# Kernel optimization log

Hardware: AMD Instinct MI355X
Metric: run time of the kernel (lower is better)

Reference implementation:

```python
import jax, jax.numpy as jnp
import numpy as np

B, H, W = 8, 64, 64
DIM_RGB, DIM_PL, EMBED, OUT = 256, 256, 128, 256
BN_EPS = 1e-5


def conv1x1(x, w, b=None):
    # x: (B,C,H,W), w: (D,C) -> (B,D,H,W)
    y = jnp.einsum('bchw,dc->bdhw', x, w)
    if b is not None:
        y = y + b[None, :, None, None]
    return y


def spatial_attention(q, k, v, scale):
    # q,k,v: (B,D,H,W)
    b, d, h, w = q.shape
    n = h * w
    qf = q.reshape(b, d, n).transpose(0, 2, 1)   # (B,N,D)
    kf = k.reshape(b, d, n)                       # (B,D,N)
    vf = v.reshape(b, d, n).transpose(0, 2, 1)   # (B,N,D)
    attn = jax.nn.softmax(jnp.einsum('bnd,bdm->bnm', qf, kf) * scale, axis=-1)
    out = jnp.einsum('bnm,bmd->bnd', attn, vf)   # (B,N,D)
    return out.transpose(0, 2, 1).reshape(b, d, h, w)


def setup_inputs() -> dict:
    key = jax.random.key(0)
    ks = jax.random.split(key, 20)
    s = 0.05
    inp = {
        'f_rgb': jax.random.normal(ks[0], (B, DIM_RGB, H, W), jnp.float32),
        'f_pl': jax.random.normal(ks[1], (B, DIM_PL, H, W), jnp.float32),
        'w_q_rgb': jax.random.normal(ks[2], (EMBED, DIM_RGB), jnp.float32) * s,
        'b_q_rgb': jax.random.normal(ks[3], (EMBED,), jnp.float32) * s,
        'w_k_pl': jax.random.normal(ks[4], (EMBED, DIM_PL), jnp.float32) * s,
        'b_k_pl': jax.random.normal(ks[5], (EMBED,), jnp.float32) * s,
        'w_v_pl': jax.random.normal(ks[6], (EMBED, DIM_PL), jnp.float32) * s,
        'b_v_pl': jax.random.normal(ks[7], (EMBED,), jnp.float32) * s,
        'w_q_pl': jax.random.normal(ks[8], (EMBED, DIM_PL), jnp.float32) * s,
        'b_q_pl': jax.random.normal(ks[9], (EMBED,), jnp.float32) * s,
        'w_k_rgb': jax.random.normal(ks[10], (EMBED, DIM_RGB), jnp.float32) * s,
        'b_k_rgb': jax.random.normal(ks[11], (EMBED,), jnp.float32) * s,
        'w_v_rgb': jax.random.normal(ks[12], (EMBED, DIM_RGB), jnp.float32) * s,
        'b_v_rgb': jax.random.normal(ks[13], (EMBED,), jnp.float32) * s,
        'w_proj': jax.random.normal(ks[14], (OUT, 2 * EMBED), jnp.float32) * s,
        'bn_gamma': jnp.ones((OUT,), jnp.float32),
        'bn_beta': jnp.zeros((OUT,), jnp.float32),
        'bn_mean': jax.random.normal(ks[15], (OUT,), jnp.float32) * 0.01,
        'bn_var': jax.random.uniform(ks[16], (OUT,), jnp.float32, 0.5, 1.5),
    }
    return inp


def reference(f_rgb, f_pl, w_q_rgb, b_q_rgb, w_k_pl, b_k_pl, w_v_pl, b_v_pl,
              w_q_pl, b_q_pl, w_k_rgb, b_k_rgb, w_v_rgb, b_v_rgb,
              w_proj, bn_gamma, bn_beta, bn_mean, bn_var):
    scale = EMBED ** -0.5
    out_rgb2pl = spatial_attention(
        conv1x1(f_rgb, w_q_rgb, b_q_rgb),
        conv1x1(f_pl, w_k_pl, b_k_pl),
        conv1x1(f_pl, w_v_pl, b_v_pl), scale)
    out_pl2rgb = spatial_attention(
        conv1x1(f_pl, w_q_pl, b_q_pl),
        conv1x1(f_rgb, w_k_rgb, b_k_rgb),
        conv1x1(f_rgb, w_v_rgb, b_v_rgb), scale)
    combined = jnp.concatenate([out_rgb2pl, out_pl2rgb], axis=1)  # (B,2E,H,W)
    y = conv1x1(combined, w_proj)  # no bias
    # BatchNorm2d (inference form) + ReLU
    inv = bn_gamma * jax.lax.rsqrt(bn_var + BN_EPS)
    y = y * inv[None, :, None, None] + (bn_beta - bn_mean * inv)[None, :, None, None]
    return jax.nn.relu(y)
```

## Files before the change

### kernel.cpp

```cpp
#include <hip/hip_runtime.h>
#include <hip/hip_bf16.h>
#include <hip/hip_fp16.h>

typedef _Float16 f16;
typedef _Float16 f16x8 __attribute__((ext_vector_type(8)));
typedef _Float16 f16x4 __attribute__((ext_vector_type(4)));
typedef float f32x4 __attribute__((ext_vector_type(4)));
typedef float f32x16 __attribute__((ext_vector_type(16)));

#define NP   4096
#define NB   8
#define CINC 256
#define EMB  128
#define OUTC 256
#define BN_EPS 1e-5f

#define DSZ  ((size_t)NB * NP * EMB)
#define TSZ  (2 * DSZ)

__global__ __launch_bounds__(256) void proj_all_kernel(
    const float* __restrict__ Xrgb, const float* __restrict__ Xpl,
    const float* __restrict__ w0, const float* __restrict__ b0,
    const float* __restrict__ w1, const float* __restrict__ b1,
    const float* __restrict__ w2, const float* __restrict__ b2,
    const float* __restrict__ w3, const float* __restrict__ b3,
    const float* __restrict__ w4, const float* __restrict__ b4,
    const float* __restrict__ w5, const float* __restrict__ b5,
    f16* __restrict__ Qt, f16* __restrict__ Kt, f16* __restrict__ Vn)
{
    const int m0 = blockIdx.x * 128;
    const int p  = blockIdx.y;
    const int b  = blockIdx.z;
    const int s  = (p >= 3) ? 1 : 0;
    const int j  = p - s * 3;
    const int tid = threadIdx.x;
    const int w = tid >> 6, lane = tid & 63, quad = lane >> 4, lr = lane & 15;

    const float* X  = s ? Xpl : Xrgb;
    const float* W  = p == 0 ? w0 : p == 1 ? w1 : p == 2 ? w2
                    : p == 3 ? w3 : p == 4 ? w4 : w5;
    const float* Bi = p == 0 ? b0 : p == 1 ? b1 : p == 2 ? b2
                    : p == 3 ? b3 : p == 4 ? b4 : b5;

    __shared__ __align__(16) f16 smem[128 * 72 * 2];
    f16* Al = smem;
    f16* Bl = smem + 128 * 72;

    f32x4 acc[2][8];
    #pragma unroll
    for (int mi = 0; mi < 2; ++mi)
        #pragma unroll
        for (int ni = 0; ni < 8; ++ni) acc[mi][ni] = (f32x4){0.f, 0.f, 0.f, 0.f};

    for (int kt = 0; kt < 4; ++kt) {
        const int kc0 = kt * 64;
        __syncthreads();
        for (int s2 = tid; s2 < 1024; s2 += 256) {
            const int n = s2 & 127, cg = s2 >> 7;
            f16 tmp[8];
            #pragma unroll
            for (int jj = 0; jj < 8; ++jj)
                tmp[jj] = (f16)X[((size_t)b * CINC + kc0 + cg * 8 + jj) * NP + m0 + n];
            *(f16x8*)&Al[n * 72 + cg * 8] = *(const f16x8*)tmp;
        }
        for (int s2 = tid; s2 < 1024; s2 += 256) {
            const int d = s2 >> 3, cg = s2 & 7;
            f16 tmp[8];
            #pragma unroll
            for (int jj = 0; jj < 8; ++jj)
                tmp[jj] = (f16)W[(size_t)d * CINC + kc0 + cg * 8 + jj];
            *(f16x8*)&Bl[d * 72 + cg * 8] = *(const f16x8*)tmp;
        }
        __syncthreads();
        #pragma unroll
        for (int ks = 0; ks < 2; ++ks) {
            f16x8 af[2], bfr[8];
            #pragma unroll
            for (int mi = 0; mi < 2; ++mi)
                af[mi] = *(const f16x8*)&Al[(w * 32 + mi * 16 + lr) * 72 + ks * 32 + quad * 8];
            #pragma unroll
            for (int ni = 0; ni < 8; ++ni)
                bfr[ni] = *(const f16x8*)&Bl[(ni * 16 + lr) * 72 + ks * 32 + quad * 8];
            #pragma unroll
            for (int mi = 0; mi < 2; ++mi)
                #pragma unroll
                for (int ni = 0; ni < 8; ++ni)
                    acc[mi][ni] = __builtin_amdgcn_mfma_f32_16x16x32_f16(
                        af[mi], bfr[ni], acc[mi][ni], 0, 0, 0);
        }
    }

    float bias[8];
    #pragma unroll
    for (int ni = 0; ni < 8; ++ni) bias[ni] = Bi[ni * 16 + lr];

    if (j < 2) {
        f16* out = (j == 0) ? (Qt + (size_t)s * DSZ) : (Kt + (size_t)(1 - s) * DSZ);
        #pragma unroll
        for (int mi = 0; mi < 2; ++mi)
            #pragma unroll
            for (int ni = 0; ni < 8; ++ni)
                #pragma unroll
                for (int r = 0; r < 4; ++r) {
                    const int n = m0 + w * 32 + mi * 16 + quad * 4 + r;
                    out[((size_t)b * NP + n) * EMB + ni * 16 + lr] =
                        (f16)(acc[mi][ni][r] + bias[ni]);
                }
    } else {
        f16* outV = Vn + (size_t)(1 - s) * DSZ;
        __syncthreads();
        f16* T = smem;
        #pragma unroll
        for (int mi = 0; mi < 2; ++mi)
            #pragma unroll
            for (int ni = 0; ni < 8; ++ni)
                #pragma unroll
                for (int r = 0; r < 4; ++r)
                    T[(ni * 16 + lr) * 136 + w * 32 + mi * 16 + quad * 4 + r] =
                        (f16)(acc[mi][ni][r] + bias[ni]);
        __syncthreads();
        for (int s2 = tid; s2 < 2048; s2 += 256) {
            const int d = s2 >> 4, n8 = (s2 & 15) * 8;
            *(f16x8*)&outV[((size_t)b * EMB + d) * NP + m0 + n8] =
                *(const f16x8*)&T[d * 136 + n8];
        }
    }
}

__device__ __forceinline__ unsigned pkf16(float a, float b) {
    union { f16 h[2]; unsigned u; } t;
    t.h[0] = (f16)a; t.h[1] = (f16)b;
    return t.u;
}

__global__ __launch_bounds__(256, 1) void attn_kernel(
    const f16* __restrict__ Qt, const f16* __restrict__ Kt,
    const f16* __restrict__ Vn, f16* __restrict__ combT)
{
    const int bid = blockIdx.x;
    const int g = bid & 15, dir = g >> 3, b = g & 7;
    const int n0 = (bid >> 4) * 256;
    const int tid = threadIdx.x;
    const int w = tid >> 6, lane = tid & 63;
    const int l31 = lane & 31, hi = lane >> 5;

    const f16* __restrict__ Q = Qt + ((size_t)dir * NB + b) * NP * EMB;
    const f16* __restrict__ K = Kt + ((size_t)dir * NB + b) * NP * EMB;
    const f16* __restrict__ V = Vn + ((size_t)dir * NB + b) * (size_t)EMB * NP;

    __shared__ __align__(16) f16 Kl[2][64 * 128];
    __shared__ __align__(16) f16 Vl[2][128 * 64];

    const int qbase = n0 + w * 64;

    f16x8 qf[2][8];
    #pragma unroll
    for (int q32 = 0; q32 < 2; ++q32)
        #pragma unroll
        for (int d16 = 0; d16 < 8; ++d16) {
            f16x8 q = *(const f16x8*)&Q[(size_t)(qbase + q32 * 32 + l31) * EMB + d16 * 16 + hi * 8];
            #pragma unroll
            for (int jj = 0; jj < 8; ++jj)
                q[jj] = q[jj] * (f16)0.12752749f;
            qf[q32][d16] = q;
        }

    f32x16 O[4][2];
    #pragma unroll
    for (int d32 = 0; d32 < 4; ++d32)
        #pragma unroll
        for (int q32 = 0; q32 < 2; ++q32) O[d32][q32] = (f32x16)(0.0f);
    float rs[2] = {0.f, 0.f};

    const int krp = lane >> 4, kp = lane & 15;
    const int vrp = lane >> 3, vp = lane & 7;
    f16x8 stK[4], stV[4];

    auto stage_load = [&](int m0) {
        #pragma unroll
        for (int i = 0; i < 4; ++i) {
            const int r = w * 16 + i * 4 + krp;
            const int c = kp ^ (r & 7);
            stK[i] = *(const f16x8*)&K[(size_t)(m0 + r) * EMB + c * 8];
        }
        #pragma unroll
        for (int i = 0; i < 4; ++i) {
            const int r = w * 32 + i * 8 + vrp;
            const int c = vp ^ (r & 7);
            stV[i] = *(const f16x8*)&V[(size_t)r * NP + m0 + c * 8];
        }
    };
    auto stage_write = [&](int buf) {
        #pragma unroll
        for (int i = 0; i < 4; ++i) {
            const int r = w * 16 + i * 4 + krp;
            *(f16x8*)&Kl[buf][r * 128 + kp * 8] = stK[i];
        }
        #pragma unroll
        for (int i = 0; i < 4; ++i) {
            const int r = w * 32 + i * 8 + vrp;
            *(f16x8*)&Vl[buf][r * 64 + vp * 8] = stV[i];
        }
    };

    stage_load(0);
    stage_write(0);
    int cur = 0;

    for (int t = 0; t < NP / 64; ++t) {
        __syncthreads();
        if (t < NP / 64 - 1) stage_load((t + 1) * 64);

        const f16* Kb = &Kl[cur][0];
        const f16* Vb = &Vl[cur][0];

        #pragma unroll
        for (int k32 = 0; k32 < 2; ++k32) {
            f32x16 s0 = (f32x16)(0.0f), s1 = (f32x16)(0.0f);
            #pragma unroll
            for (int d16 = 0; d16 < 8; ++d16) {
                const int r = k32 * 32 + l31;
                const int c = (d16 * 2 + hi) ^ (r & 7);
                const f16x8 kf = *(const f16x8*)&Kb[r * 128 + c * 8];
                s0 = __builtin_amdgcn_mfma_f32_32x32x16_f16(kf, qf[0][d16], s0, 0, 0, 0);
                s1 = __builtin_amdgcn_mfma_f32_32x32x16_f16(kf, qf[1][d16], s1, 0, 0, 0);
            }

            f16x8 pb[2][2];
            #pragma unroll
            for (int q32 = 0; q32 < 2; ++q32) {
                const f32x16 s = q32 ? s1 : s0;
                float e[16];
                #pragma unroll
                for (int i = 0; i < 16; ++i) e[i] = __builtin_amdgcn_exp2f(s[i]);
                float sum = 0.f;
                #pragma unroll
                for (int i = 0; i < 16; ++i) sum += e[i];
                rs[q32] += sum;
                #pragma unroll
                for (int g2 = 0; g2 < 2; ++g2) {
                    const unsigned pa  = pkf16(e[g2 * 8 + 0], e[g2 * 8 + 1]);
                    const unsigned pbu = pkf16(e[g2 * 8 + 2], e[g2 * 8 + 3]);
                    const unsigned pc  = pkf16(e[g2 * 8 + 4], e[g2 * 8 + 5]);
                    const unsigned pd  = pkf16(e[g2 * 8 + 6], e[g2 * 8 + 7]);
                    const unsigned recv0 = __shfl_xor(hi ? pa : pc, 32);
                    const unsigned recv1 = __shfl_xor(hi ? pbu : pd, 32);
                    union { unsigned u[4]; f16x8 v; } pu;
                    pu.u[0] = hi ? recv0 : pa;
                    pu.u[1] = hi ? recv1 : pbu;
                    pu.u[2] = hi ? pc : recv0;
                    pu.u[3] = hi ? pd : recv1;
                    pb[g2][q32] = pu.v;
                }
            }

            #pragma unroll
            for (int g2 = 0; g2 < 2; ++g2) {
                #pragma unroll
                for (int d32 = 0; d32 < 4; ++d32) {
                    const int r = d32 * 32 + l31;
                    const int c = ((k32 * 2 + g2) * 2 + hi) ^ (r & 7);
                    const f16x8 vf = *(const f16x8*)&Vb[r * 64 + c * 8];
                    O[d32][0] = __builtin_amdgcn_mfma_f32_32x32x16_f16(vf, pb[g2][0], O[d32][0], 0, 0, 0);
                    O[d32][1] = __builtin_amdgcn_mfma_f32_32x32x16_f16(vf, pb[g2][1], O[d32][1], 0, 0, 0);
                }
            }
        }

        if (t < NP / 64 - 1) stage_write(cur ^ 1);
        cur ^= 1;
    }

    rs[0] += __shfl_xor(rs[0], 32);
    rs[1] += __shfl_xor(rs[1], 32);
    const float inv[2] = {1.0f / rs[0], 1.0f / rs[1]};
    #pragma unroll
    for (int q32 = 0; q32 < 2; ++q32) {
        const int n = qbase + q32 * 32 + l31;
        #pragma unroll
        for (int d32 = 0; d32 < 4; ++d32)
            #pragma unroll
            for (int tq = 0; tq < 4; ++tq) {
                f16 o4[4];
                #pragma unroll
                for (int jj = 0; jj < 4; ++jj)
                    o4[jj] = (f16)(O[d32][q32][tq * 4 + jj] * inv[q32]);
                *(f16x4*)&combT[((size_t)b * NP + n) * OUTC + dir * EMB + d32 * 32 + tq * 8 + hi * 4] =
                    *(const f16x4*)o4;
            }
    }
}

__global__ __launch_bounds__(256) void proj_out_kernel(
    const f16* __restrict__ combT, const float* __restrict__ Wp,
    const float* __restrict__ G, const float* __restrict__ Be,
    const float* __restrict__ Mu, const float* __restrict__ Va,
    float* __restrict__ out)
{
    const int m0 = blockIdx.x * 128;
    const int o0 = blockIdx.y * 128;
    const int b  = blockIdx.z;
    const int tid = threadIdx.x;
    const int w = tid >> 6, lane = tid & 63, quad = lane >> 4, lr = lane & 15;

    __shared__ __align__(16) f16 smem[128 * 72 * 2];
    f16* Al = smem;
    f16* Bl = smem + 128 * 72;

    f32x4 acc[2][8];
    #pragma unroll
    for (int mi = 0; mi < 2; ++mi)
        #pragma unroll
        for (int ni = 0; ni < 8; ++ni) acc[mi][ni] = (f32x4){0.f, 0.f, 0.f, 0.f};

    for (int kt = 0; kt < 4; ++kt) {
        const int kc0 = kt * 64;
        __syncthreads();
        #pragma unroll
        for (int i = 0; i < 4; ++i) {
            const int s2 = i * 256 + tid;
            const int n = s2 >> 3, cg = s2 & 7;
            *(f16x8*)&Al[n * 72 + cg * 8] =
                *(const f16x8*)&combT[((size_t)b * NP + m0 + n) * OUTC + kc0 + cg * 8];
        }
        for (int s2 = tid; s2 < 1024; s2 += 256) {
            const int d = s2 >> 3, cg = s2 & 7;
            f16 tmp[8];
            #pragma unroll
            for (int jj = 0; jj < 8; ++jj)
                tmp[jj] = (f16)Wp[(size_t)(o0 + d) * OUTC + kc0 + cg * 8 + jj];
            *(f16x8*)&Bl[d * 72 + cg * 8] = *(const f16x8*)tmp;
        }
        __syncthreads();
        #pragma unroll
        for (int ks = 0; ks < 2; ++ks) {
            f16x8 af[2], bfr[8];
            #pragma unroll
            for (int mi = 0; mi < 2; ++mi)
                af[mi] = *(const f16x8*)&Al[(w * 32 + mi * 16 + lr) * 72 + ks * 32 + quad * 8];
            #pragma unroll
            for (int ni = 0; ni < 8; ++ni)
                bfr[ni] = *(const f16x8*)&Bl[(ni * 16 + lr) * 72 + ks * 32 + quad * 8];
            #pragma unroll
            for (int mi = 0; mi < 2; ++mi)
                #pragma unroll
                for (int ni = 0; ni < 8; ++ni)
                    acc[mi][ni] = __builtin_amdgcn_mfma_f32_16x16x32_f16(
                        af[mi], bfr[ni], acc[mi][ni], 0, 0, 0);
        }
    }

    __syncthreads();
    f16* T = smem;
    #pragma unroll
    for (int ni = 0; ni < 8; ++ni) {
        const int o = o0 + ni * 16 + lr;
        const float iv = G[o] * rsqrtf(Va[o] + BN_EPS);
        const float sh = Be[o] - Mu[o] * iv;
        #pragma unroll
        for (int mi = 0; mi < 2; ++mi)
            #pragma unroll
            for (int r = 0; r < 4; ++r)
                T[(ni * 16 + lr) * 136 + w * 32 + mi * 16 + quad * 4 + r] =
                    (f16)fmaxf(acc[mi][ni][r] * iv + sh, 0.f);
    }
    __syncthreads();
    for (int s2 = tid; s2 < 2048; s2 += 256) {
        const int o = s2 >> 4, n8 = (s2 & 15) * 8;
        const f16x8 v = *(const f16x8*)&T[o * 136 + n8];
        const size_t off = ((size_t)b * OUTC + o0 + o) * NP + m0 + n8;
        #pragma unroll
        for (int k = 0; k < 8; ++k) out[off + k] = (float)v[k];
    }
}

extern "C" void kernel_launch(void* const* d_in, const int* in_sizes, int n_in,
                              void* d_out, int out_size, void* d_ws, size_t ws_size,
                              hipStream_t stream) {
    const float* f_rgb   = (const float*)d_in[0];
    const float* f_pl    = (const float*)d_in[1];
    const float* w_q_rgb = (const float*)d_in[2];  const float* b_q_rgb = (const float*)d_in[3];
    const float* w_k_pl  = (const float*)d_in[4];  const float* b_k_pl  = (const float*)d_in[5];
    const float* w_v_pl  = (const float*)d_in[6];  const float* b_v_pl  = (const float*)d_in[7];
    const float* w_q_pl  = (const float*)d_in[8];  const float* b_q_pl  = (const float*)d_in[9];
    const float* w_k_rgb = (const float*)d_in[10]; const float* b_k_rgb = (const float*)d_in[11];
    const float* w_v_rgb = (const float*)d_in[12]; const float* b_v_rgb = (const float*)d_in[13];
    const float* w_proj  = (const float*)d_in[14];
    const float* bn_g    = (const float*)d_in[15]; const float* bn_b = (const float*)d_in[16];
    const float* bn_m    = (const float*)d_in[17]; const float* bn_v = (const float*)d_in[18];

    f16* Qt    = (f16*)d_ws;
    f16* Kt    = Qt + TSZ;
    f16* Vn    = Kt + TSZ;
    f16* combT = Vn + TSZ;

    proj_all_kernel<<<dim3(32, 6, 8), 256, 0, stream>>>(
        f_rgb, f_pl,
        w_q_rgb, b_q_rgb, w_k_rgb, b_k_rgb, w_v_rgb, b_v_rgb,
        w_q_pl,  b_q_pl,  w_k_pl,  b_k_pl,  w_v_pl,  b_v_pl,
        Qt, Kt, Vn);

    attn_kernel<<<256, 256, 0, stream>>>(Qt, Kt, Vn, combT);

    proj_out_kernel<<<dim3(32, 2, 8), 256, 0, stream>>>(
        combT, w_proj, bn_g, bn_b, bn_m, bn_v, (float*)d_out);
}
```

Measured before the change: 372.6 us.

## Halve attention query tile per wave, double grid, permute V layout to drop shuffles

Each attention wave now handles 32 queries instead of 64, and the grid doubles to 512 blocks with launch bounds allowing two blocks per CU, cutting register pressure so more waves can hide latency. The V projection store permutes quad order so that the P fragment built from exp values already matches the MFMA B-operand layout, which removes the cross-half shuffles in favour of packed cvt_pkrtz conversions. s_setprio is raised around the MFMA blocks to favour matrix issue. In exchange, each K/V tile loaded into LDS is reused by half as many queries, which doubles total K/V traffic through global memory and LDS.

```diff
diff --git a/kernel.cpp b/kernel.cpp
--- a/kernel.cpp
+++ b/kernel.cpp
@@ -5,6 +5,7 @@
 typedef _Float16 f16;
 typedef _Float16 f16x8 __attribute__((ext_vector_type(8)));
 typedef _Float16 f16x4 __attribute__((ext_vector_type(4)));
+typedef __fp16 hf16x2 __attribute__((ext_vector_type(2)));
 typedef float f32x4 __attribute__((ext_vector_type(4)));
 typedef float f32x16 __attribute__((ext_vector_type(16)));
 
@@ -110,13 +111,14 @@
         f16* outV = Vn + (size_t)(1 - s) * DSZ;
         __syncthreads();
         f16* T = smem;
+        const int quad_p = ((quad & 1) << 1) | (quad >> 1);
         #pragma unroll
         for (int mi = 0; mi < 2; ++mi)
             #pragma unroll
             for (int ni = 0; ni < 8; ++ni)
                 #pragma unroll
                 for (int r = 0; r < 4; ++r)
-                    T[(ni * 16 + lr) * 136 + w * 32 + mi * 16 + quad * 4 + r] =
+                    T[(ni * 16 + lr) * 136 + w * 32 + mi * 16 + quad_p * 4 + r] =
                         (f16)(acc[mi][ni][r] + bias[ni]);
         __syncthreads();
         for (int s2 = tid; s2 < 2048; s2 += 256) {
@@ -127,19 +129,13 @@
     }
 }
 
-__device__ __forceinline__ unsigned pkf16(float a, float b) {
-    union { f16 h[2]; unsigned u; } t;
-    t.h[0] = (f16)a; t.h[1] = (f16)b;
-    return t.u;
-}
-
-__global__ __launch_bounds__(256, 1) void attn_kernel(
+__global__ __launch_bounds__(256, 2) void attn_kernel(
     const f16* __restrict__ Qt, const f16* __restrict__ Kt,
     const f16* __restrict__ Vn, f16* __restrict__ combT)
 {
     const int bid = blockIdx.x;
     const int g = bid & 15, dir = g >> 3, b = g & 7;
-    const int n0 = (bid >> 4) * 256;
+    const int n0 = (bid >> 4) * 128;
     const int tid = threadIdx.x;
     const int w = tid >> 6, lane = tid & 63;
     const int l31 = lane & 31, hi = lane >> 5;
@@ -151,26 +147,22 @@
     __shared__ __align__(16) f16 Kl[2][64 * 128];
     __shared__ __align__(16) f16 Vl[2][128 * 64];
 
-    const int qbase = n0 + w * 64;
-
-    f16x8 qf[2][8];
-    #pragma unroll
-    for (int q32 = 0; q32 < 2; ++q32)
-        #pragma unroll
-        for (int d16 = 0; d16 < 8; ++d16) {
-            f16x8 q = *(const f16x8*)&Q[(size_t)(qbase + q32 * 32 + l31) * EMB + d16 * 16 + hi * 8];
-            #pragma unroll
-            for (int jj = 0; jj < 8; ++jj)
-                q[jj] = q[jj] * (f16)0.12752749f;
-            qf[q32][d16] = q;
-        }
-
-    f32x16 O[4][2];
-    #pragma unroll
-    for (int d32 = 0; d32 < 4; ++d32)
-        #pragma unroll
-        for (int q32 = 0; q32 < 2; ++q32) O[d32][q32] = (f32x16)(0.0f);
-    float rs[2] = {0.f, 0.f};
+    const int qbase = n0 + w * 32;
+
+    f16x8 qf[8];
+    #pragma unroll
+    for (int d16 = 0; d16 < 8; ++d16) {
+        f16x8 q = *(const f16x8*)&Q[(size_t)(qbase + l31) * EMB + d16 * 16 + hi * 8];
+        #pragma unroll
+        for (int jj = 0; jj < 8; ++jj)
+            q[jj] = q[jj] * (f16)0.12752749f;
+        qf[d16] = q;
+    }
+
+    f32x16 O[4];
+    #pragma unroll
+    for (int d32 = 0; d32 < 4; ++d32) O[d32] = (f32x16)(0.0f);
+    float rs = 0.f;
 
     const int krp = lane >> 4, kp = lane & 15;
     const int vrp = lane >> 3, vp = lane & 7;
@@ -216,79 +208,67 @@
 
         #pragma unroll
         for (int k32 = 0; k32 < 2; ++k32) {
-            f32x16 s0 = (f32x16)(0.0f), s1 = (f32x16)(0.0f);
+            f32x16 s = (f32x16)(0.0f);
+            __builtin_amdgcn_s_setprio(1);
             #pragma unroll
             for (int d16 = 0; d16 < 8; ++d16) {
                 const int r = k32 * 32 + l31;
                 const int c = (d16 * 2 + hi) ^ (r & 7);
                 const f16x8 kf = *(const f16x8*)&Kb[r * 128 + c * 8];
-                s0 = __builtin_amdgcn_mfma_f32_32x32x16_f16(kf, qf[0][d16], s0, 0, 0, 0);
-                s1 = __builtin_amdgcn_mfma_f32_32x32x16_f16(kf, qf[1][d16], s1, 0, 0, 0);
+                s = __builtin_amdgcn_mfma_f32_32x32x16_f16(kf, qf[d16], s, 0, 0, 0);
             }
-
-            f16x8 pb[2][2];
-            #pragma unroll
-            for (int q32 = 0; q32 < 2; ++q32) {
-                const f32x16 s = q32 ? s1 : s0;
-                float e[16];
-                #pragma unroll
-                for (int i = 0; i < 16; ++i) e[i] = __builtin_amdgcn_exp2f(s[i]);
-                float sum = 0.f;
-                #pragma unroll
-                for (int i = 0; i < 16; ++i) sum += e[i];
-                rs[q32] += sum;
-                #pragma unroll
-                for (int g2 = 0; g2 < 2; ++g2) {
-                    const unsigned pa  = pkf16(e[g2 * 8 + 0], e[g2 * 8 + 1]);
-                    const unsigned pbu = pkf16(e[g2 * 8 + 2], e[g2 * 8 + 3]);
-                    const unsigned pc  = pkf16(e[g2 * 8 + 4], e[g2 * 8 + 5]);
-                    const unsigned pd  = pkf16(e[g2 * 8 + 6], e[g2 * 8 + 7]);
-                    const unsigned recv0 = __shfl_xor(hi ? pa : pc, 32);
-                    const unsigned recv1 = __shfl_xor(hi ? pbu : pd, 32);
-                    union { unsigned u[4]; f16x8 v; } pu;
-                    pu.u[0] = hi ? recv0 : pa;
-                    pu.u[1] = hi ? recv1 : pbu;
-                    pu.u[2] = hi ? pc : recv0;
-                    pu.u[3] = hi ? pd : recv1;
-                    pb[g2][q32] = pu.v;
+            __builtin_amdgcn_s_setprio(0);
+
+            float e[16];
+            #pragma unroll
+            for (int i = 0; i < 16; ++i) e[i] = __builtin_amdgcn_exp2f(s[i]);
+            float sum = 0.f;
+            #pragma unroll
+            for (int i = 0; i < 16; ++i) sum += e[i];
+            rs += sum;
+            f16x8 pb[2];
+            #pragma unroll
+            for (int g2 = 0; g2 < 2; ++g2) {
+                union { hf16x2 h[4]; f16x8 v; } pu;
+                #pragma unroll
+                for (int t2 = 0; t2 < 4; ++t2)
+                    pu.h[t2] = __builtin_amdgcn_cvt_pkrtz(e[g2 * 8 + t2 * 2],
+                                                          e[g2 * 8 + t2 * 2 + 1]);
+                pb[g2] = pu.v;
+            }
+
+            __builtin_amdgcn_s_setprio(1);
+            #pragma unroll
+            for (int g2 = 0; g2 < 2; ++g2) {
+                #pragma unroll
+                for (int d32 = 0; d32 < 4; ++d32) {
+                    const int r = d32 * 32 + l31;
+                    const int c = (k32 * 4 + g2 * 2 + hi) ^ (r & 7);
+                    const f16x8 vf = *(const f16x8*)&Vb[r * 64 + c * 8];
+                    O[d32] = __builtin_amdgcn_mfma_f32_32x32x16_f16(vf, pb[g2], O[d32], 0, 0, 0);
                 }
             }
-
-            #pragma unroll
-            for (int g2 = 0; g2 < 2; ++g2) {
-                #pragma unroll
-                for (int d32 = 0; d32 < 4; ++d32) {
-                    const int r = d32 * 32 + l31;
-                    const int c = ((k32 * 2 + g2) * 2 + hi) ^ (r & 7);
-                    const f16x8 vf = *(const f16x8*)&Vb[r * 64 + c * 8];
-                    O[d32][0] = __builtin_amdgcn_mfma_f32_32x32x16_f16(vf, pb[g2][0], O[d32][0], 0, 0, 0);
-                    O[d32][1] = __builtin_amdgcn_mfma_f32_32x32x16_f16(vf, pb[g2][1], O[d32][1], 0, 0, 0);
-                }
-            }
+            __builtin_amdgcn_s_setprio(0);
         }
 
         if (t < NP / 64 - 1) stage_write(cur ^ 1);
         cur ^= 1;
     }
 
-    rs[0] += __shfl_xor(rs[0], 32);
-    rs[1] += __shfl_xor(rs[1], 32);
-    const float inv[2] = {1.0f / rs[0], 1.0f / rs[1]};
-    #pragma unroll
-    for (int q32 = 0; q32 < 2; ++q32) {
-        const int n = qbase + q32 * 32 + l31;
-        #pragma unroll
-        for (int d32 = 0; d32 < 4; ++d32)
-            #pragma unroll
-            for (int tq = 0; tq < 4; ++tq) {
-                f16 o4[4];
-                #pragma unroll
-                for (int jj = 0; jj < 4; ++jj)
-                    o4[jj] = (f16)(O[d32][q32][tq * 4 + jj] * inv[q32]);
-                *(f16x4*)&combT[((size_t)b * NP + n) * OUTC + dir * EMB + d32 * 32 + tq * 8 + hi * 4] =
-                    *(const f16x4*)o4;
-            }
-    }
+    rs += __shfl_xor(rs, 32);
+    const float inv = 1.0f / rs;
+    const int n = qbase + l31;
+    #pragma unroll
+    for (int d32 = 0; d32 < 4; ++d32)
+        #pragma unroll
+        for (int tq = 0; tq < 4; ++tq) {
+            f16 o4[4];
+            #pragma unroll
+            for (int jj = 0; jj < 4; ++jj)
+                o4[jj] = (f16)(O[d32][tq * 4 + jj] * inv);
+            *(f16x4*)&combT[((size_t)b * NP + n) * OUTC + dir * EMB + d32 * 32 + tq * 8 + hi * 4] =
+                *(const f16x4*)o4;
+        }
 }
 
 __global__ __launch_bounds__(256) void proj_out_kernel(
@@ -400,7 +380,7 @@
         w_q_pl,  b_q_pl,  w_k_pl,  b_k_pl,  w_v_pl,  b_v_pl,
         Qt, Kt, Vn);
 
-    attn_kernel<<<256, 256, 0, stream>>>(Qt, Kt, Vn, combT);
+    attn_kernel<<<512, 256, 0, stream>>>(Qt, Kt, Vn, combT);
 
     proj_out_kernel<<<dim3(32, 2, 8), 256, 0, stream>>>(
         combT, w_proj, bn_g, bn_b, bn_m, bn_v, (float*)d_out);
```

Measured after the change: 347.5 us. -6.8%, faster.

## Split attention keys across warp pairs, double grid, and merge partial sums

Applied to the files above, without the earlier changes.

The attention kernel now gives each block 128 queries instead of 256, with two warps per query group. Each warp of a pair handles half of the key sequence, and the two partial outputs and row sums are merged through shared memory at the end. The grid doubles to 512 blocks with two blocks per CU allowed. The V layout produced by the projection kernel is permuted so the P fragments can be packed directly with cvt_pkrtz, which removes the cross-lane shuffles. MFMA sections are also wrapped in s_setprio. The aim is more parallelism and occupancy and less shuffle overhead, at the cost of a split-K reduction and less K/V reuse per block.

```diff
diff --git a/kernel.cpp b/kernel.cpp
--- a/kernel.cpp
+++ b/kernel.cpp
@@ -5,6 +5,7 @@
 typedef _Float16 f16;
 typedef _Float16 f16x8 __attribute__((ext_vector_type(8)));
 typedef _Float16 f16x4 __attribute__((ext_vector_type(4)));
+typedef __fp16 hf16x2 __attribute__((ext_vector_type(2)));
 typedef float f32x4 __attribute__((ext_vector_type(4)));
 typedef float f32x16 __attribute__((ext_vector_type(16)));
 
@@ -110,13 +111,14 @@
         f16* outV = Vn + (size_t)(1 - s) * DSZ;
         __syncthreads();
         f16* T = smem;
+        const int quad_p = ((quad & 1) << 1) | (quad >> 1);
         #pragma unroll
         for (int mi = 0; mi < 2; ++mi)
             #pragma unroll
             for (int ni = 0; ni < 8; ++ni)
                 #pragma unroll
                 for (int r = 0; r < 4; ++r)
-                    T[(ni * 16 + lr) * 136 + w * 32 + mi * 16 + quad * 4 + r] =
+                    T[(ni * 16 + lr) * 136 + w * 32 + mi * 16 + quad_p * 4 + r] =
                         (f16)(acc[mi][ni][r] + bias[ni]);
         __syncthreads();
         for (int s2 = tid; s2 < 2048; s2 += 256) {
@@ -127,31 +129,28 @@
     }
 }
 
-__device__ __forceinline__ unsigned pkf16(float a, float b) {
-    union { f16 h[2]; unsigned u; } t;
-    t.h[0] = (f16)a; t.h[1] = (f16)b;
-    return t.u;
-}
-
-__global__ __launch_bounds__(256, 1) void attn_kernel(
+__global__ __launch_bounds__(256, 2) void attn_kernel(
     const f16* __restrict__ Qt, const f16* __restrict__ Kt,
     const f16* __restrict__ Vn, f16* __restrict__ combT)
 {
     const int bid = blockIdx.x;
     const int g = bid & 15, dir = g >> 3, b = g & 7;
-    const int n0 = (bid >> 4) * 256;
+    const int n0 = (bid >> 4) * 128;
     const int tid = threadIdx.x;
     const int w = tid >> 6, lane = tid & 63;
     const int l31 = lane & 31, hi = lane >> 5;
+    const int qsub = w >> 1;
+    const int kh   = w & 1;
 
     const f16* __restrict__ Q = Qt + ((size_t)dir * NB + b) * NP * EMB;
     const f16* __restrict__ K = Kt + ((size_t)dir * NB + b) * NP * EMB;
     const f16* __restrict__ V = Vn + ((size_t)dir * NB + b) * (size_t)EMB * NP;
 
-    __shared__ __align__(16) f16 Kl[2][64 * 128];
-    __shared__ __align__(16) f16 Vl[2][128 * 64];
-
-    const int qbase = n0 + w * 64;
+    __shared__ __align__(16) f16 Kl[2][2][32 * 128];
+    __shared__ __align__(16) f16 Vl[2][2][128 * 40];
+
+    const int qbase = n0 + qsub * 64;
+    const int m00 = kh * 2048;
 
     f16x8 qf[2][8];
     #pragma unroll
@@ -173,33 +172,33 @@
     float rs[2] = {0.f, 0.f};
 
     const int krp = lane >> 4, kp = lane & 15;
-    const int vrp = lane >> 3, vp = lane & 7;
+    const int vrp = lane >> 2, vp = lane & 3;
     f16x8 stK[4], stV[4];
 
-    auto stage_load = [&](int m0) {
+    auto stage_load = [&](int t) {
+        const int mk = m00 + t * 32;
         #pragma unroll
         for (int i = 0; i < 4; ++i) {
-            const int r = w * 16 + i * 4 + krp;
+            const int r = qsub * 16 + i * 4 + krp;
             const int c = kp ^ (r & 7);
-            stK[i] = *(const f16x8*)&K[(size_t)(m0 + r) * EMB + c * 8];
+            stK[i] = *(const f16x8*)&K[(size_t)(mk + r) * EMB + c * 8];
         }
         #pragma unroll
         for (int i = 0; i < 4; ++i) {
-            const int r = w * 32 + i * 8 + vrp;
-            const int c = vp ^ (r & 7);
-            stV[i] = *(const f16x8*)&V[(size_t)r * NP + m0 + c * 8];
+            const int rd = qsub * 64 + i * 16 + vrp;
+            stV[i] = *(const f16x8*)&V[(size_t)rd * NP + mk + vp * 8];
         }
     };
     auto stage_write = [&](int buf) {
         #pragma unroll
         for (int i = 0; i < 4; ++i) {
-            const int r = w * 16 + i * 4 + krp;
-            *(f16x8*)&Kl[buf][r * 128 + kp * 8] = stK[i];
+            const int r = qsub * 16 + i * 4 + krp;
+            *(f16x8*)&Kl[kh][buf][r * 128 + kp * 8] = stK[i];
         }
         #pragma unroll
         for (int i = 0; i < 4; ++i) {
-            const int r = w * 32 + i * 8 + vrp;
-            *(f16x8*)&Vl[buf][r * 64 + vp * 8] = stV[i];
+            const int rd = qsub * 64 + i * 16 + vrp;
+            *(f16x8*)&Vl[kh][buf][rd * 40 + vp * 8] = stV[i];
         }
     };
 
@@ -207,87 +206,109 @@
     stage_write(0);
     int cur = 0;
 
-    for (int t = 0; t < NP / 64; ++t) {
-        __syncthreads();
-        if (t < NP / 64 - 1) stage_load((t + 1) * 64);
-
-        const f16* Kb = &Kl[cur][0];
-        const f16* Vb = &Vl[cur][0];
-
-        #pragma unroll
-        for (int k32 = 0; k32 < 2; ++k32) {
-            f32x16 s0 = (f32x16)(0.0f), s1 = (f32x16)(0.0f);
-            #pragma unroll
-            for (int d16 = 0; d16 < 8; ++d16) {
-                const int r = k32 * 32 + l31;
-                const int c = (d16 * 2 + hi) ^ (r & 7);
-                const f16x8 kf = *(const f16x8*)&Kb[r * 128 + c * 8];
-                s0 = __builtin_amdgcn_mfma_f32_32x32x16_f16(kf, qf[0][d16], s0, 0, 0, 0);
-                s1 = __builtin_amdgcn_mfma_f32_32x32x16_f16(kf, qf[1][d16], s1, 0, 0, 0);
+    for (int t = 0; t < 64; ++t) {
+        __syncthreads();
+        if (t < 63) stage_load(t + 1);
+
+        const f16* Kb = &Kl[kh][cur][0];
+        const f16* Vb = &Vl[kh][cur][0];
+
+        f32x16 s0 = (f32x16)(0.0f), s1 = (f32x16)(0.0f);
+        __builtin_amdgcn_s_setprio(1);
+        #pragma unroll
+        for (int d16 = 0; d16 < 8; ++d16) {
+            const int c = (d16 * 2 + hi) ^ (l31 & 7);
+            const f16x8 kf = *(const f16x8*)&Kb[l31 * 128 + c * 8];
+            s0 = __builtin_amdgcn_mfma_f32_32x32x16_f16(kf, qf[0][d16], s0, 0, 0, 0);
+            s1 = __builtin_amdgcn_mfma_f32_32x32x16_f16(kf, qf[1][d16], s1, 0, 0, 0);
+        }
+        __builtin_amdgcn_s_setprio(0);
+
+        f16x8 pb[2][2];
+        #pragma unroll
+        for (int q32 = 0; q32 < 2; ++q32) {
+            const f32x16 s = q32 ? s1 : s0;
+            float e[16];
+            #pragma unroll
+            for (int i = 0; i < 16; ++i) e[i] = __builtin_amdgcn_exp2f(s[i]);
+            float sum = 0.f;
+            #pragma unroll
+            for (int i = 0; i < 16; ++i) sum += e[i];
+            rs[q32] += sum;
+            #pragma unroll
+            for (int g2 = 0; g2 < 2; ++g2) {
+                union { hf16x2 h[4]; f16x8 v; } pu;
+                #pragma unroll
+                for (int t2 = 0; t2 < 4; ++t2)
+                    pu.h[t2] = __builtin_amdgcn_cvt_pkrtz(e[g2 * 8 + t2 * 2],
+                                                          e[g2 * 8 + t2 * 2 + 1]);
+                pb[g2][q32] = pu.v;
             }
-
-            f16x8 pb[2][2];
-            #pragma unroll
-            for (int q32 = 0; q32 < 2; ++q32) {
-                const f32x16 s = q32 ? s1 : s0;
-                float e[16];
-                #pragma unroll
-                for (int i = 0; i < 16; ++i) e[i] = __builtin_amdgcn_exp2f(s[i]);
-                float sum = 0.f;
-                #pragma unroll
-                for (int i = 0; i < 16; ++i) sum += e[i];
-                rs[q32] += sum;
-                #pragma unroll
-                for (int g2 = 0; g2 < 2; ++g2) {
-                    const unsigned pa  = pkf16(e[g2 * 8 + 0], e[g2 * 8 + 1]);
-                    const unsigned pbu = pkf16(e[g2 * 8 + 2], e[g2 * 8 + 3]);
-                    const unsigned pc  = pkf16(e[g2 * 8 + 4], e[g2 * 8 + 5]);
-                    const unsigned pd  = pkf16(e[g2 * 8 + 6], e[g2 * 8 + 7]);
-                    const unsigned recv0 = __shfl_xor(hi ? pa : pc, 32);
-                    const unsigned recv1 = __shfl_xor(hi ? pbu : pd, 32);
-                    union { unsigned u[4]; f16x8 v; } pu;
-                    pu.u[0] = hi ? recv0 : pa;
-                    pu.u[1] = hi ? recv1 : pbu;
-                    pu.u[2] = hi ? pc : recv0;
-                    pu.u[3] = hi ? pd : recv1;
-                    pb[g2][q32] = pu.v;
-                }
+        }
+
+        __builtin_amdgcn_s_setprio(1);
+        #pragma unroll
+        for (int g2 = 0; g2 < 2; ++g2) {
+            #pragma unroll
+            for (int d32 = 0; d32 < 4; ++d32) {
+                const f16x8 vf = *(const f16x8*)&Vb[(d32 * 32 + l31) * 40 + (g2 * 2 + hi) * 8];
+                O[d32][0] = __builtin_amdgcn_mfma_f32_32x32x16_f16(vf, pb[g2][0], O[d32][0], 0, 0, 0);
+                O[d32][1] = __builtin_amdgcn_mfma_f32_32x32x16_f16(vf, pb[g2][1], O[d32][1], 0, 0, 0);
             }
-
-            #pragma unroll
-            for (int g2 = 0; g2 < 2; ++g2) {
-                #pragma unroll
-                for (int d32 = 0; d32 < 4; ++d32) {
-                    const int r = d32 * 32 + l31;
-                    const int c = ((k32 * 2 + g2) * 2 + hi) ^ (r & 7);
-                    const f16x8 vf = *(const f16x8*)&Vb[r * 64 + c * 8];
-                    O[d32][0] = __builtin_amdgcn_mfma_f32_32x32x16_f16(vf, pb[g2][0], O[d32][0], 0, 0, 0);
-                    O[d32][1] = __builtin_amdgcn_mfma_f32_32x32x16_f16(vf, pb[g2][1], O[d32][1], 0, 0, 0);
-                }
-            }
-        }
-
-        if (t < NP / 64 - 1) stage_write(cur ^ 1);
+        }
+        __builtin_amdgcn_s_setprio(0);
+
+        if (t < 63) stage_write(cur ^ 1);
         cur ^= 1;
     }
 
     rs[0] += __shfl_xor(rs[0], 32);
     rs[1] += __shfl_xor(rs[1], 32);
-    const float inv[2] = {1.0f / rs[0], 1.0f / rs[1]};
-    #pragma unroll
-    for (int q32 = 0; q32 < 2; ++q32) {
-        const int n = qbase + q32 * 32 + l31;
-        #pragma unroll
-        for (int d32 = 0; d32 < 4; ++d32)
-            #pragma unroll
-            for (int tq = 0; tq < 4; ++tq) {
-                f16 o4[4];
-                #pragma unroll
-                for (int jj = 0; jj < 4; ++jj)
-                    o4[jj] = (f16)(O[d32][q32][tq * 4 + jj] * inv[q32]);
-                *(f16x4*)&combT[((size_t)b * NP + n) * OUTC + dir * EMB + d32 * 32 + tq * 8 + hi * 4] =
-                    *(const f16x4*)o4;
-            }
+
+    __syncthreads();
+    f16*   Xch = (f16*)&Kl[0][0][0];
+    float* rsX = (float*)&Vl[0][0][0];
+
+    if (kh == 1) {
+        #pragma unroll
+        for (int q32 = 0; q32 < 2; ++q32) {
+            const float inv = 1.0f / rs[q32];
+            const int ql = qsub * 64 + q32 * 32 + l31;
+            #pragma unroll
+            for (int d32 = 0; d32 < 4; ++d32)
+                #pragma unroll
+                for (int tq = 0; tq < 4; ++tq) {
+                    f16 o4[4];
+                    #pragma unroll
+                    for (int jj = 0; jj < 4; ++jj)
+                        o4[jj] = (f16)(O[d32][q32][tq * 4 + jj] * inv);
+                    *(f16x4*)&Xch[ql * 128 + d32 * 32 + tq * 8 + hi * 4] = *(const f16x4*)o4;
+                }
+            if (hi == 0) rsX[ql] = rs[q32];
+        }
+    }
+    __syncthreads();
+    if (kh == 0) {
+        #pragma unroll
+        for (int q32 = 0; q32 < 2; ++q32) {
+            const int ql = qsub * 64 + q32 * 32 + l31;
+            const float rs1 = rsX[ql];
+            const float wt = 1.0f / (rs[q32] + rs1);
+            const float w1 = rs1 * wt;
+            const int n = qbase + q32 * 32 + l31;
+            #pragma unroll
+            for (int d32 = 0; d32 < 4; ++d32)
+                #pragma unroll
+                for (int tq = 0; tq < 4; ++tq) {
+                    const f16x4 oh = *(const f16x4*)&Xch[ql * 128 + d32 * 32 + tq * 8 + hi * 4];
+                    f16 o4[4];
+                    #pragma unroll
+                    for (int jj = 0; jj < 4; ++jj)
+                        o4[jj] = (f16)(O[d32][q32][tq * 4 + jj] * wt + (float)oh[jj] * w1);
+                    *(f16x4*)&combT[((size_t)b * NP + n) * OUTC + dir * EMB + d32 * 32 + tq * 8 + hi * 4] =
+                        *(const f16x4*)o4;
+                }
+        }
     }
 }
 
@@ -400,7 +421,7 @@
         w_q_pl,  b_q_pl,  w_k_pl,  b_k_pl,  w_v_pl,  b_v_pl,
         Qt, Kt, Vn);
 
-    attn_kernel<<<256, 256, 0, stream>>>(Qt, Kt, Vn, combT);
+    attn_kernel<<<512, 256, 0, stream>>>(Qt, Kt, Vn, combT);
 
     proj_out_kernel<<<dim3(32, 2, 8), 256, 0, stream>>>(
         combT, w_proj, bn_g, bn_b, bn_m, bn_v, (float*)d_out);
```

New measurement: 463.9 us. 1.24x slower.
